# Performance work log

Measured on AMD Instinct MI355X. Metric: run time of the kernel, lower is better.

Reference implementation:

```python
import jax, jax.numpy as jnp
import numpy as np

N_NODES = 50000; N_INTRA = 800000; N_INTER = 400000; N_IEDGE = 600000
N_GRAPHS = 128; F_IN = 54; DIM = 128; N_GNN = 3; DIM_MLP = 128
DEV_VDW_COEFF = 0.2; EPS_LO = 0.0178; EPS_HI = 0.2
VDW_N_SHORT = 10.0; VDW_N_LONG = 6.0
RANGE_LO = 0.5; RANGE_HI = 5.0
HBOND_CUT = (-0.7, 0.0); METAL_CUT = (-0.7, 0.0); HYDRO_CUT = (0.5, 1.5)


def _lin(key, fi, fo):
    return jax.random.normal(key, (fi, fo), jnp.float32) / np.float32(np.sqrt(fi))


def setup_inputs():
    key = jax.random.key(0)
    ks = iter(jax.random.split(key, 48))
    nk = lambda: next(ks)
    inp = {}
    inp['x'] = jax.random.normal(nk(), (N_NODES, F_IN), jnp.float32)
    inp['pos'] = jax.random.uniform(nk(), (N_NODES, 3), jnp.float32, 0.0, 20.0)
    inp['vdw_radii'] = jax.random.uniform(nk(), (N_NODES,), jnp.float32, 1.0, 2.0)
    inp['rotor'] = jax.random.randint(nk(), (N_GRAPHS, 1), 0, 20).astype(jnp.float32)
    inp['edge_index'] = jax.random.randint(nk(), (2, N_INTRA), 0, N_NODES)
    inp['edge_index_c'] = jax.random.randint(nk(), (2, N_INTER), 0, N_NODES)
    inp['edge_index_i'] = jax.random.randint(nk(), (2, N_IEDGE), 0, N_NODES)
    inp['batch'] = jnp.sort(jax.random.randint(nk(), (N_NODES,), 0, N_GRAPHS))
    for name, p in (('is_metal', 0.02), ('is_h_donor', 0.15), ('is_h_acceptor', 0.2), ('is_hydrophobic', 0.4)):
        inp[name] = jax.random.bernoulli(nk(), p, (N_NODES,))
    inp['embed_W'] = _lin(nk(), F_IN, DIM)
    inp['gat_W'] = jax.random.normal(nk(), (N_GNN, DIM, DIM), jnp.float32) / np.float32(np.sqrt(DIM))
    inp['gat_Wb'] = jnp.zeros((N_GNN, DIM), jnp.float32)
    inp['gat_A'] = 0.1 * jax.random.normal(nk(), (N_GNN, DIM, DIM), jnp.float32) / np.float32(np.sqrt(DIM))
    inp['gat_gate_w'] = jax.random.normal(nk(), (N_GNN, 2 * DIM, 1), jnp.float32) / np.float32(np.sqrt(2 * DIM))
    inp['gat_gate_b'] = jnp.zeros((N_GNN, 1), jnp.float32)
    inp['inter_W'] = jax.random.normal(nk(), (N_GNN, DIM, DIM), jnp.float32) / np.float32(np.sqrt(DIM))
    inp['inter_Wb'] = jnp.zeros((N_GNN, DIM), jnp.float32)
    inp['inter_gate_w'] = jax.random.normal(nk(), (N_GNN, 2 * DIM, 1), jnp.float32) / np.float32(np.sqrt(2 * DIM))
    inp['inter_gate_b'] = jnp.zeros((N_GNN, 1), jnp.float32)
    inp['eps_w1'] = _lin(nk(), 2 * DIM, DIM_MLP); inp['eps_b1'] = jnp.zeros((DIM_MLP,), jnp.float32)
    inp['eps_w2'] = _lin(nk(), DIM_MLP, 1); inp['eps_b2'] = jnp.zeros((1,), jnp.float32)
    inp['dvdw_w1'] = _lin(nk(), 2 * DIM, DIM_MLP); inp['dvdw_b1'] = jnp.zeros((DIM_MLP,), jnp.float32)
    inp['dvdw_w2'] = _lin(nk(), DIM_MLP, 1); inp['dvdw_b2'] = jnp.zeros((1,), jnp.float32)
    inp['hbond_coeff'] = jnp.array([1.0], jnp.float32)
    inp['hydrophobic_coeff'] = jnp.array([0.5], jnp.float32)
    inp['rotor_coeff'] = jnp.array([0.5], jnp.float32)
    return inp


def _gated_gat(x, src, dst, W, Wb, A, gw, gb):
    n = x.shape[0]
    h = x @ W + Wb                                   # [N, D]
    logits = jnp.sum((h @ A)[dst] * h[src], axis=-1)  # per-edge attention logit
    mx = jax.ops.segment_max(logits, dst, num_segments=n)
    mx = jnp.where(jnp.isfinite(mx), mx, 0.0)
    ex = jnp.exp(logits - mx[dst])
    den = jax.ops.segment_sum(ex, dst, num_segments=n)
    alpha = ex / (den[dst] + 1e-16)                  # segment softmax over incoming edges
    h_prime = jax.nn.relu(jax.ops.segment_sum(alpha[:, None] * h[src], dst, num_segments=n))
    z = jax.nn.sigmoid(jnp.concatenate([x, h_prime], -1) @ gw + gb)
    return z * x + (1.0 - z) * h_prime


def _interaction(x, src, dst, W, Wb, gw, gb):
    n = x.shape[0]
    m = jax.ops.segment_sum(jax.nn.relu(x[src] @ W + Wb), dst, num_segments=n)
    z = jax.nn.sigmoid(jnp.concatenate([x, m], -1) @ gw + gb)
    return z * x + (1.0 - z) * m


def _lj(D, R, eps, n_short, n_long):
    dr = jnp.maximum(D / R, 0.5)  # numerical clamp mirroring PIGNet's distance clamp
    n = jnp.where(dr < 1.0, n_short, n_long)
    return eps * (dr ** (-2.0 * n) - 2.0 * dr ** (-n))


def _linear_potential(D, R, minima, c_short, c_long):
    frac = jnp.clip(((D - R) - c_long) / (c_short - c_long), 0.0, 1.0)
    return minima * frac


def _forward(x, pos, vdw_radii, rotor, embed_W, gat_W, gat_Wb, gat_A, gat_gate_w, gat_gate_b,
             inter_W, inter_Wb, inter_gate_w, inter_gate_b,
             eps_w1, eps_b1, eps_w2, eps_b2, dvdw_w1, dvdw_b1, dvdw_w2, dvdw_b2,
             hbond_coeff, hydrophobic_coeff, rotor_coeff,
             edge_index, edge_index_c, edge_index_i, batch,
             is_metal, is_h_donor, is_h_acceptor, is_hydrophobic):
    h = x @ embed_W
    for l in range(N_GNN):
        h = _gated_gat(h, edge_index[0], edge_index[1], gat_W[l], gat_Wb[l], gat_A[l], gat_gate_w[l], gat_gate_b[l])
    for l in range(N_GNN):
        h = _interaction(h, edge_index_c[0], edge_index_c[1], inter_W[l], inter_Wb[l], inter_gate_w[l], inter_gate_b[l])
    i, j = edge_index_i[0], edge_index_i[1]
    diff = pos[i] - pos[j]
    D = jnp.sqrt(jnp.sum(diff * diff, axis=-1) + 1e-10)           # [E]
    rmask = ((D >= RANGE_LO) & (D <= RANGE_HI)).astype(h.dtype)
    x_cat = jnp.concatenate([h[i], h[j]], axis=-1)                # [E, 2*DIM]
    dvdw = jnp.tanh(jax.nn.relu(x_cat @ dvdw_w1 + dvdw_b1) @ dvdw_w2 + dvdw_b2)[:, 0]
    dvdw = dvdw * DEV_VDW_COEFF * rmask
    R = vdw_radii[i] + vdw_radii[j] + dvdw
    eps = jax.nn.sigmoid(jax.nn.relu(x_cat @ eps_w1 + eps_b1) @ eps_w2 + eps_b2)[:, 0]
    eps = eps * (EPS_HI - EPS_LO) + EPS_LO
    min_hb = -hbond_coeff ** 2
    min_hp = -hydrophobic_coeff ** 2
    e = jnp.stack([
        _lj(D, R, eps, VDW_N_SHORT, VDW_N_LONG),
        _linear_potential(D, R, min_hb, *HBOND_CUT),
        _linear_potential(D, R, min_hb, *METAL_CUT),
        _linear_potential(D, R, min_hp, *HYDRO_CUT),
    ])                                                            # [4, E]
    no_metal = ~(is_metal[i] | is_metal[j])
    masks = jnp.stack([
        no_metal,
        ((is_h_donor[i] & is_h_acceptor[j]) | (is_h_acceptor[i] & is_h_donor[j])) & no_metal,
        (is_metal[i] & is_h_acceptor[j]) | (is_h_acceptor[i] & is_metal[j]),
        is_hydrophobic[i] & is_hydrophobic[j] & no_metal,
    ]).astype(e.dtype)
    e = e * masks * rmask
    energies = jax.ops.segment_sum(e.T, batch[i], num_segments=N_GRAPHS)  # [G, 4]
    penalty = 1.0 + rotor_coeff ** 2 * rotor                               # [G, 1]
    return energies / penalty, dvdw


def reference(x, pos, vdw_radii, rotor, edge_index, edge_index_c, edge_index_i, batch,
              is_metal, is_h_donor, is_h_acceptor, is_hydrophobic,
              embed_W, gat_W, gat_Wb, gat_A, gat_gate_w, gat_gate_b,
              inter_W, inter_Wb, inter_gate_w, inter_gate_b,
              eps_w1, eps_b1, eps_w2, eps_b2, dvdw_w1, dvdw_b1, dvdw_w2, dvdw_b2,
              hbond_coeff, hydrophobic_coeff, rotor_coeff):
    return _forward(x, pos, vdw_radii, rotor, embed_W, gat_W, gat_Wb, gat_A, gat_gate_w, gat_gate_b,
                    inter_W, inter_Wb, inter_gate_w, inter_gate_b,
                    eps_w1, eps_b1, eps_w2, eps_b2, dvdw_w1, dvdw_b1, dvdw_w2, dvdw_b2,
                    hbond_coeff, hydrophobic_coeff, rotor_coeff,
                    edge_index, edge_index_c, edge_index_i, batch,
                    is_metal, is_h_donor, is_h_acceptor, is_hydrophobic)
```

## Files before the change

kernel.cpp:

```cpp
#include <hip/hip_runtime.h>
#include <math.h>

#define NN 50000
#define EA 800000
#define EC 400000
#define EIN 600000
#define NG 128
#define FIN 54

#define DEV_VDW 0.2f
#define EPS_LO_ 0.0178f
#define EPS_HI_ 0.2f

typedef unsigned int uint;
typedef unsigned short ushort;
typedef unsigned long long ull;
typedef __attribute__((ext_vector_type(8))) short bf16x8;
typedef __attribute__((ext_vector_type(4))) float f32x4;

__device__ __forceinline__ ushort f2bf(float f){
  uint x = __float_as_uint(f);
  uint r = x + 0x7fffu + ((x >> 16) & 1u);
  return (ushort)(r >> 16);
}
__device__ __forceinline__ uint f2bf2(float a, float b){
  return (uint)f2bf(a) | ((uint)f2bf(b) << 16);
}
__device__ __forceinline__ void decode8(uint4 u, float* f){
  f[0] = __uint_as_float(u.x << 16); f[1] = __uint_as_float(u.x & 0xffff0000u);
  f[2] = __uint_as_float(u.y << 16); f[3] = __uint_as_float(u.y & 0xffff0000u);
  f[4] = __uint_as_float(u.z << 16); f[5] = __uint_as_float(u.z & 0xffff0000u);
  f[6] = __uint_as_float(u.w << 16); f[7] = __uint_as_float(u.w & 0xffff0000u);
}

__global__ void k_rank(const int* __restrict__ dstA, const int* __restrict__ dstC,
                       const int* __restrict__ dstI,
                       int* __restrict__ cntA, int* __restrict__ cntC, int* __restrict__ cntI,
                       int* __restrict__ rnkA, int* __restrict__ rnkC, int* __restrict__ rnkI){
  int b = blockIdx.x;
  const int* dst; int* cnt; int* rnk; int E; int bid; int nb;
  if (b < 1024){ dst = dstA; cnt = cntA; rnk = rnkA; E = EA;  bid = b;        nb = 1024; }
  else if (b < 1536){ dst = dstC; cnt = cntC; rnk = rnkC; E = EC;  bid = b - 1024; nb = 512; }
  else { dst = dstI; cnt = cntI; rnk = rnkI; E = EIN; bid = b - 1536; nb = 1024; }
  for (int i = bid * 256 + threadIdx.x; i < E; i += nb * 256)
    rnk[i] = atomicAdd(&cnt[dst[i]], 1);
}

__global__ void k_scan3(const int* __restrict__ cntA, int* __restrict__ offA,
                        const int* __restrict__ cntC, int* __restrict__ offC,
                        const int* __restrict__ cntI, int* __restrict__ offI){
  const int* cnt = (blockIdx.x == 0) ? cntA : (blockIdx.x == 1) ? cntC : cntI;
  int* off = (blockIdx.x == 0) ? offA : (blockIdx.x == 1) ? offC : offI;
  int n = NN;
  __shared__ int wsums[16];
  __shared__ int run_s;
  int tid = threadIdx.x;
  int lane = tid & 63, w = tid >> 6;
  if (tid == 0) run_s = 0;
  __syncthreads();
  for (int base = 0; base < n; base += 1024){
    int run = run_s;
    int i = base + tid;
    int v = (i < n) ? cnt[i] : 0;
    int s = v;
    #pragma unroll
    for (int o = 1; o < 64; o <<= 1){ int t = __shfl_up(s, o, 64); if (lane >= o) s += t; }
    if (lane == 63) wsums[w] = s;
    __syncthreads();
    if (w == 0 && lane < 16){
      int t = wsums[lane];
      #pragma unroll
      for (int o = 1; o < 16; o <<= 1){ int u = __shfl_up(t, o, 64); if (lane >= o) t += u; }
      wsums[lane] = t;
    }
    __syncthreads();
    int woff = (w == 0) ? 0 : wsums[w - 1];
    int excl = run + woff + (s - v);
    if (i < n) off[i] = excl;
    int tot = wsums[15];
    __syncthreads();
    if (tid == 0) run_s = run + tot;
    __syncthreads();
  }
  if (threadIdx.x == 0) off[n] = run_s;
}

__global__ void k_place(const int* __restrict__ eiA, const int* __restrict__ eiC,
                        const int* __restrict__ eiI,
                        const int* __restrict__ offA, const int* __restrict__ rnkA, int* __restrict__ srcA,
                        const int* __restrict__ offC, const int* __restrict__ rnkC, int* __restrict__ srcC,
                        const int* __restrict__ offI, const int* __restrict__ rnkI, ull* __restrict__ jeI){
  int b = blockIdx.x;
  if (b < 1024){
    for (int i = b * 256 + threadIdx.x; i < EA; i += 1024 * 256){
      int d = eiA[EA + i];
      __builtin_nontemporal_store(eiA[i], &srcA[offA[d] + rnkA[i]]);
    }
  } else if (b < 1536){
    int bid = b - 1024;
    for (int i = bid * 256 + threadIdx.x; i < EC; i += 512 * 256){
      int d = eiC[EC + i];
      __builtin_nontemporal_store(eiC[i], &srcC[offC[d] + rnkC[i]]);
    }
  } else {
    int bid = b - 1536;
    for (int i = bid * 256 + threadIdx.x; i < EIN; i += 1024 * 256){
      int key = eiI[i];
      ull v = ((ull)(uint)i << 32) | (uint)eiI[EIN + i];
      __builtin_nontemporal_store(v, &jeI[offI[key] + rnkI[i]]);
    }
  }
}

__global__ void k_nodeinfo(const float* __restrict__ POS, const float* __restrict__ RAD,
                           const int* __restrict__ Mmet, const int* __restrict__ Mdon,
                           const int* __restrict__ Macc, const int* __restrict__ Mhyd,
                           const int* __restrict__ BATCH,
                           float4* __restrict__ PRAD, uint* __restrict__ MB){
  int n = blockIdx.x * 256 + threadIdx.x;
  if (n < NN){
    PRAD[n] = make_float4(POS[3*n], POS[3*n+1], POS[3*n+2], RAD[n]);
    uint m = (Mmet[n] ? 1u : 0u) | (Mdon[n] ? 2u : 0u) | (Macc[n] ? 4u : 0u) |
             (Mhyd[n] ? 8u : 0u) | ((uint)BATCH[n] << 8);
    MB[n] = m;
  }
}

__global__ __launch_bounds__(256) void k_prepw(const float* __restrict__ gatW, const float* __restrict__ gatA,
                        const float* __restrict__ intW, const float* __restrict__ dw1,
                        const float* __restrict__ ew1,
                        const float* __restrict__ gatWb, const float* __restrict__ intWb,
                        const float* __restrict__ db1, const float* __restrict__ eb1,
                        uint* __restrict__ Wt, float* __restrict__ BIASALL){
  __shared__ ushort L[128 * 132];
  int m = blockIdx.x;
  int tid = threadIdx.x;
  if (m == 13){
    for (int idx = tid; idx < 13 * 128; idx += 256){
      int slot = idx >> 7, c = idx & 127;
      if (slot >= 3 && slot < 6) continue;
      float v = 0.f;
      if (slot < 3) v = gatWb[slot * 128 + c];
      else if (slot < 9) v = intWb[(slot - 6) * 128 + c];
      else if (slot == 9) v = db1[c];
      else if (slot == 11) v = eb1[c];
      BIASALL[idx] = v;
    }
    return;
  }
  if (m >= 3 && m < 6){
    int l = m - 3;
    const float* Wf  = gatW + l * 16384;
    const float* Af  = gatA + l * 16384;
    const float* Wbf = gatWb + l * 128;
    for (int idx = tid; idx < 16384; idx += 256){
      int k = idx >> 7, n = idx & 127;
      L[k * 132 + n] = f2bf(Af[idx]);
    }
    __syncthreads();
    int r = tid >> 1, ch = tid & 1;
    float accv[64];
    #pragma unroll
    for (int c = 0; c < 64; ++c) accv[c] = 0.f;
    float accb = 0.f;
    int bc = tid & 127;
    for (int mm = 0; mm < 128; ++mm){
      float wv = Wf[r * 128 + mm];
      const uint* Lr32 = (const uint*)&L[mm * 132 + ch * 64];
      #pragma unroll
      for (int c2 = 0; c2 < 32; ++c2){
        uint u = Lr32[c2];
        accv[2 * c2]     += wv * __uint_as_float(u << 16);
        accv[2 * c2 + 1] += wv * __uint_as_float(u & 0xffff0000u);
      }
      accb += Wbf[mm] * __uint_as_float((uint)L[mm * 132 + bc] << 16);
    }
    __syncthreads();
    #pragma unroll
    for (int c = 0; c < 64; ++c) L[r * 132 + ch * 64 + c] = f2bf(accv[c]);
    if (tid < 128) BIASALL[(3 + l) * 128 + tid] = accb;
    __syncthreads();
    int n = tid & 127, half = tid >> 7;
    uint* outp = Wt + (size_t)m * 8192 + n * 64 + half * 32;
    #pragma unroll
    for (int kk2 = 0; kk2 < 32; ++kk2){
      int k = half * 64 + 2 * kk2;
      uint u = (uint)L[k * 132 + n] | ((uint)L[(k + 1) * 132 + n] << 16);
      outp[kk2] = u;
    }
    return;
  }
  const float* src = (m < 3)  ? gatW + m * 16384 :
                     (m < 9)  ? intW + (m - 6) * 16384 :
                     (m < 11) ? dw1 + (m - 9) * 16384 :
                                ew1 + (m - 11) * 16384;
  for (int idx = tid; idx < 16384; idx += 256){
    int k = idx >> 7, n = idx & 127;
    L[k * 132 + n] = f2bf(src[idx]);
  }
  __syncthreads();
  int n = tid & 127, half = tid >> 7;
  uint* outp = Wt + (size_t)m * 8192 + n * 64 + half * 32;
  #pragma unroll
  for (int kk2 = 0; kk2 < 32; ++kk2){
    int k = half * 64 + 2 * kk2;
    uint u = (uint)L[k * 132 + n] | ((uint)L[(k + 1) * 132 + n] << 16);
    outp[kk2] = u;
  }
}

__global__ void k_embed(const float* __restrict__ X, const float* __restrict__ W,
                        uint* __restrict__ Hh){
  __shared__ float Wls[FIN * 128];
  int tid = threadIdx.x;
  for (int i = tid; i < FIN * 128; i += 128) Wls[i] = W[i];
  __syncthreads();
  for (int row = blockIdx.x; row < NN; row += gridDim.x){
    const float* xr = X + row * FIN;
    float acc = 0.f;
    #pragma unroll
    for (int k = 0; k < FIN; ++k) acc += xr[k] * Wls[k * 128 + tid];
    ((ushort*)Hh)[(size_t)row * 128 + tid] = f2bf(acc);
  }
}

template<bool RELU>
__global__ __launch_bounds__(256) void k_gemm_mfma(const uint* __restrict__ Ah,
        const uint* __restrict__ Bt0, size_t strideB,
        const float* __restrict__ bias0, size_t strideBias,
        uint* __restrict__ C0, size_t strideC, int N){
  const uint* Bt = Bt0 + (size_t)blockIdx.y * strideB;
  const float* bias = bias0 + (size_t)blockIdx.y * strideBias;
  uint* Cout = C0 + (size_t)blockIdx.y * strideC;
  int tid = threadIdx.x;
  int lane = tid & 63;
  int wv = tid >> 6;
  int row0 = blockIdx.x * 128 + wv * 32;
  int l15 = lane & 15, lg = lane >> 4;
  int ra0 = row0 + l15, ra1 = row0 + 16 + l15;
  const uint* pa0 = Ah + (size_t)(ra0 < N ? ra0 : 0) * 64 + lg * 4;
  const uint* pa1 = Ah + (size_t)(ra1 < N ? ra1 : 0) * 64 + lg * 4;
  const uint* pb  = Bt + (size_t)l15 * 64 + lg * 4;
  f32x4 acc[2][8] = {};
  #pragma unroll
  for (int c = 0; c < 4; ++c){
    bf16x8 a0 = *(const bf16x8*)(pa0 + c * 16);
    bf16x8 a1 = *(const bf16x8*)(pa1 + c * 16);
    #pragma unroll
    for (int ct = 0; ct < 8; ++ct){
      bf16x8 b = *(const bf16x8*)(pb + ct * 1024 + c * 16);
      acc[0][ct] = __builtin_amdgcn_mfma_f32_16x16x32_bf16(a0, b, acc[0][ct], 0, 0, 0);
      acc[1][ct] = __builtin_amdgcn_mfma_f32_16x16x32_bf16(a1, b, acc[1][ct], 0, 0, 0);
    }
  }
  #pragma unroll
  for (int ct = 0; ct < 8; ++ct){
    int col = ct * 16 + l15;
    float bv = bias[col];
    #pragma unroll
    for (int rt = 0; rt < 2; ++rt){
      int rbase = row0 + rt * 16 + lg * 4;
      f32x4 a4 = acc[rt][ct];
      #pragma unroll
      for (int r = 0; r < 4; ++r){
        int row = rbase + r;
        if (row < N){
          float t = a4[r] + bv;
          if (RELU) t = fmaxf(t, 0.f);
          ((ushort*)Cout)[(size_t)row * 128 + col] = f2bf(t);
        }
      }
    }
  }
}

__global__ __launch_bounds__(256) void k_gat(uint* __restrict__ Hh,
                      const uint* __restrict__ HWh, const uint* __restrict__ HAh,
                      const int* __restrict__ off, const int* __restrict__ srcs,
                      const float* __restrict__ GW, const float* __restrict__ GB){
  int tid = threadIdx.x;
  int sub = tid & 15;
  int n = blockIdx.x * 16 + (tid >> 4);
  if (n >= NN) return;
  uint4 au = *(const uint4*)(HAh + (size_t)n * 64 + sub * 4);
  float a[8]; decode8(au, a);
  int e0 = off[n], deg = off[n + 1] - e0;
  float m = -INFINITY, den = 0.f;
  float acc[8] = {};
  uint4 w0v = {}, w1v = {}, w2v = {};
  if (deg > 0) w0v = *(const uint4*)(HWh + (size_t)srcs[e0] * 64 + sub * 4);
  if (deg > 1) w1v = *(const uint4*)(HWh + (size_t)srcs[e0 + 1] * 64 + sub * 4);
  if (deg > 2) w2v = *(const uint4*)(HWh + (size_t)srcs[e0 + 2] * 64 + sub * 4);
  for (int t = 0; t < deg; ++t){
    uint4 wn = {};
    if (t + 3 < deg) wn = *(const uint4*)(HWh + (size_t)srcs[e0 + t + 3] * 64 + sub * 4);
    float w[8]; decode8(w0v, w);
    float p = a[0]*w[0] + a[1]*w[1] + a[2]*w[2] + a[3]*w[3]
            + a[4]*w[4] + a[5]*w[5] + a[6]*w[6] + a[7]*w[7];
    #pragma unroll
    for (int o = 8; o; o >>= 1) p += __shfl_xor(p, o, 64);
    float mn = fmaxf(m, p);
    float cf = __expf(m - mn);
    float ex = __expf(p - mn);
    den = den * cf + ex;
    #pragma unroll
    for (int q = 0; q < 8; ++q) acc[q] = acc[q] * cf + ex * w[q];
    m = mn;
    w0v = w1v; w1v = w2v; w2v = wn;
  }
  float inv = 1.f / (den + 1e-16f);
  float hp[8];
  #pragma unroll
  for (int q = 0; q < 8; ++q) hp[q] = fmaxf(acc[q] * inv, 0.f);
  uint4 xu = *(const uint4*)(Hh + (size_t)n * 64 + sub * 4);
  float x[8]; decode8(xu, x);
  float gx[8], gh[8];
  *(float4*)&gx[0] = *(const float4*)(GW + sub * 8);
  *(float4*)&gx[4] = *(const float4*)(GW + sub * 8 + 4);
  *(float4*)&gh[0] = *(const float4*)(GW + 128 + sub * 8);
  *(float4*)&gh[4] = *(const float4*)(GW + 128 + sub * 8 + 4);
  float g = 0.f;
  #pragma unroll
  for (int q = 0; q < 8; ++q) g += x[q] * gx[q] + hp[q] * gh[q];
  #pragma unroll
  for (int o = 8; o; o >>= 1) g += __shfl_xor(g, o, 64);
  g += GB[0];
  float z = 1.f / (1.f + __expf(-g));
  #pragma unroll
  for (int q = 0; q < 8; ++q) x[q] = z * x[q] + (1.f - z) * hp[q];
  uint4 hw;
  hw.x = f2bf2(x[0], x[1]); hw.y = f2bf2(x[2], x[3]);
  hw.z = f2bf2(x[4], x[5]); hw.w = f2bf2(x[6], x[7]);
  *(uint4*)(Hh + (size_t)n * 64 + sub * 4) = hw;
}

__global__ __launch_bounds__(256) void k_inter(uint* __restrict__ Hh,
                        const uint* __restrict__ Th,
                        const int* __restrict__ off, const int* __restrict__ srcs,
                        const float* __restrict__ GW, const float* __restrict__ GB){
  int tid = threadIdx.x;
  int sub = tid & 15;
  int n = blockIdx.x * 16 + (tid >> 4);
  if (n >= NN) return;
  int e0 = off[n], deg = off[n + 1] - e0;
  float acc[8] = {};
  uint4 w0v = {}, w1v = {}, w2v = {};
  if (deg > 0) w0v = *(const uint4*)(Th + (size_t)srcs[e0] * 64 + sub * 4);
  if (deg > 1) w1v = *(const uint4*)(Th + (size_t)srcs[e0 + 1] * 64 + sub * 4);
  if (deg > 2) w2v = *(const uint4*)(Th + (size_t)srcs[e0 + 2] * 64 + sub * 4);
  for (int t = 0; t < deg; ++t){
    uint4 wn = {};
    if (t + 3 < deg) wn = *(const uint4*)(Th + (size_t)srcs[e0 + t + 3] * 64 + sub * 4);
    float w[8]; decode8(w0v, w);
    #pragma unroll
    for (int q = 0; q < 8; ++q) acc[q] += w[q];
    w0v = w1v; w1v = w2v; w2v = wn;
  }
  uint4 xu = *(const uint4*)(Hh + (size_t)n * 64 + sub * 4);
  float x[8]; decode8(xu, x);
  float gx[8], gh[8];
  *(float4*)&gx[0] = *(const float4*)(GW + sub * 8);
  *(float4*)&gx[4] = *(const float4*)(GW + sub * 8 + 4);
  *(float4*)&gh[0] = *(const float4*)(GW + 128 + sub * 8);
  *(float4*)&gh[4] = *(const float4*)(GW + 128 + sub * 8 + 4);
  float g = 0.f;
  #pragma unroll
  for (int q = 0; q < 8; ++q) g += x[q] * gx[q] + acc[q] * gh[q];
  #pragma unroll
  for (int o = 8; o; o >>= 1) g += __shfl_xor(g, o, 64);
  g += GB[0];
  float z = 1.f / (1.f + __expf(-g));
  #pragma unroll
  for (int q = 0; q < 8; ++q) x[q] = z * x[q] + (1.f - z) * acc[q];
  uint4 hw;
  hw.x = f2bf2(x[0], x[1]); hw.y = f2bf2(x[2], x[3]);
  hw.z = f2bf2(x[4], x[5]); hw.w = f2bf2(x[6], x[7]);
  *(uint4*)(Hh + (size_t)n * 64 + sub * 4) = hw;
}

__global__ __launch_bounds__(256) void k_edges(
    const int* __restrict__ offI, const ull* __restrict__ jeI,
    const float4* __restrict__ PRAD, const uint* __restrict__ MB,
    const uint* __restrict__ Pd, const uint* __restrict__ Qd,
    const uint* __restrict__ Pe, const uint* __restrict__ Qe,
    const float* __restrict__ w2d, const float* __restrict__ b2d,
    const float* __restrict__ w2e, const float* __restrict__ b2e,
    const float* __restrict__ hbc, const float* __restrict__ hpc,
    float* __restrict__ geng, float* __restrict__ outdv){
  int tid = threadIdx.x;
  int sub = tid & 15;
  int n = blockIdx.x * 16 + (tid >> 4);
  if (n >= NN) return;
  int e0 = offI[n], deg = offI[n + 1] - e0;
  if (deg == 0) return;
  float wdv[8], wev[8];
  *(float4*)&wdv[0] = *(const float4*)(w2d + sub * 8);
  *(float4*)&wdv[4] = *(const float4*)(w2d + sub * 8 + 4);
  *(float4*)&wev[0] = *(const float4*)(w2e + sub * 8);
  *(float4*)&wev[4] = *(const float4*)(w2e + sub * 8 + 4);
  float bd = b2d[0], be = b2e[0];
  float minhb = -hbc[0] * hbc[0], minhp = -hpc[0] * hpc[0];
  uint4 pdu = *(const uint4*)(Pd + (size_t)n * 64 + sub * 4);
  uint4 peu = *(const uint4*)(Pe + (size_t)n * 64 + sub * 4);
  float pdf[8], pef[8];
  decode8(pdu, pdf); decode8(peu, pef);
  float4 pri = PRAD[n];
  uint mbi = MB[n];
  float E0 = 0.f, E1 = 0.f, E2 = 0.f, E3 = 0.f;

  ull je0 = jeI[e0];
  int j0 = (int)(uint)je0;
  uint4 qd0 = *(const uint4*)(Qd + (size_t)j0 * 64 + sub * 4);
  uint4 qe0 = *(const uint4*)(Qe + (size_t)j0 * 64 + sub * 4);
  float4 prj0 = PRAD[j0];
  uint mbj0 = MB[j0];

  for (int t = 0; t < deg; ++t){
    ull je1 = 0; uint4 qd1 = {}, qe1 = {}; float4 prj1 = {}; uint mbj1 = 0;
    if (t + 1 < deg){
      je1 = jeI[e0 + t + 1];
      int j1 = (int)(uint)je1;
      qd1 = *(const uint4*)(Qd + (size_t)j1 * 64 + sub * 4);
      qe1 = *(const uint4*)(Qe + (size_t)j1 * 64 + sub * 4);
      prj1 = PRAD[j1]; mbj1 = MB[j1];
    }
    float qdf[8], qef[8];
    decode8(qd0, qdf); decode8(qe0, qef);
    float sd = 0.f, se = 0.f;
    #pragma unroll
    for (int q = 0; q < 8; ++q){
      sd += fmaxf(pdf[q] + qdf[q], 0.f) * wdv[q];
      se += fmaxf(pef[q] + qef[q], 0.f) * wev[q];
    }
    #pragma unroll
    for (int o = 8; o; o >>= 1){
      sd += __shfl_xor(sd, o, 64);
      se += __shfl_xor(se, o, 64);
    }
    sd += bd; se += be;
    float dx = pri.x - prj0.x, dy = pri.y - prj0.y, dz = pri.z - prj0.z;
    float D = sqrtf(dx * dx + dy * dy + dz * dz + 1e-10f);
    float rmask = (D >= 0.5f && D <= 5.0f) ? 1.f : 0.f;
    float ex2 = __expf(2.f * fminf(sd, 15.f));
    float th = __fdividef(ex2 - 1.f, ex2 + 1.f);
    float dvdw = th * DEV_VDW * rmask;
    float eps = __fdividef(1.f, 1.f + __expf(-se)) * (EPS_HI_ - EPS_LO_) + EPS_LO_;
    float R = pri.w + prj0.w + dvdw;
    float dr = fmaxf(__fdividef(D, R), 0.5f);
    float nn2 = (dr < 1.f) ? 10.f : 6.f;
    float tp = __expf(-nn2 * __logf(dr));
    float ev = eps * (tp * tp - 2.f * tp);
    float dmr = D - R;
    float f1 = fminf(fmaxf(dmr * (-1.f / 0.7f), 0.f), 1.f);
    float f3 = fminf(fmaxf(1.5f - dmr, 0.f), 1.f);
    bool metI = mbi & 1, metJ = mbj0 & 1;
    bool donI = mbi & 2, donJ = mbj0 & 2;
    bool accI = mbi & 4, accJ = mbj0 & 4;
    bool hyI  = mbi & 8, hyJ  = mbj0 & 8;
    bool nm = !(metI || metJ);
    if (sub == 0) __builtin_nontemporal_store(dvdw, &outdv[(int)(je0 >> 32)]);
    E0 += nm ? ev * rmask : 0.f;
    E1 += (((donI && accJ) || (accI && donJ)) && nm) ? minhb * f1 * rmask : 0.f;
    E2 += ((metI && accJ) || (accI && metJ)) ? minhb * f1 * rmask : 0.f;
    E3 += (hyI && hyJ && nm) ? minhp * f3 * rmask : 0.f;
    je0 = je1; qd0 = qd1; qe0 = qe1; prj0 = prj1; mbj0 = mbj1;
  }
  if (sub == 0){
    float* part = geng + (size_t)(blockIdx.x & 7) * (NG * 4);
    int g = (int)(mbi >> 8) * 4;
    atomicAdd(&part[g + 0], E0);
    atomicAdd(&part[g + 1], E1);
    atomicAdd(&part[g + 2], E2);
    atomicAdd(&part[g + 3], E3);
  }
}

__global__ void k_final(const float* __restrict__ geng, const float* __restrict__ rotor,
                        const float* __restrict__ rc, float* __restrict__ out){
  int t = blockIdx.x * blockDim.x + threadIdx.x;
  if (t < NG * 4){
    int g = t >> 2;
    float s = 0.f;
    #pragma unroll
    for (int p = 0; p < 8; ++p) s += geng[p * NG * 4 + t];
    float pen = 1.f + rc[0] * rc[0] * rotor[g];
    out[t] = s / pen;
  }
}

extern "C" void kernel_launch(void* const* d_in, const int* in_sizes, int n_in,
                              void* d_out, int out_size, void* d_ws, size_t ws_size,
                              hipStream_t stream){
  (void)in_sizes; (void)n_in; (void)out_size; (void)ws_size;
  const float* X    = (const float*)d_in[0];
  const float* POS  = (const float*)d_in[1];
  const float* RAD  = (const float*)d_in[2];
  const float* ROT  = (const float*)d_in[3];
  const int* EIa    = (const int*)d_in[4];
  const int* EIc    = (const int*)d_in[5];
  const int* EIi    = (const int*)d_in[6];
  const int* BATCH  = (const int*)d_in[7];
  const int* Mmet = (const int*)d_in[8];
  const int* Mdon = (const int*)d_in[9];
  const int* Macc = (const int*)d_in[10];
  const int* Mhyd = (const int*)d_in[11];
  const float* embW  = (const float*)d_in[12];
  const float* gatW  = (const float*)d_in[13];
  const float* gatWb = (const float*)d_in[14];
  const float* gatA  = (const float*)d_in[15];
  const float* gatGw = (const float*)d_in[16];
  const float* gatGb = (const float*)d_in[17];
  const float* intW  = (const float*)d_in[18];
  const float* intWb = (const float*)d_in[19];
  const float* intGw = (const float*)d_in[20];
  const float* intGb = (const float*)d_in[21];
  const float* ew1 = (const float*)d_in[22];
  const float* eb1 = (const float*)d_in[23];
  const float* ew2 = (const float*)d_in[24];
  const float* eb2 = (const float*)d_in[25];
  const float* dw1 = (const float*)d_in[26];
  const float* db1 = (const float*)d_in[27];
  const float* dw2 = (const float*)d_in[28];
  const float* db2 = (const float*)d_in[29];
  const float* hbc = (const float*)d_in[30];
  const float* hpc = (const float*)d_in[31];
  const float* rcc = (const float*)d_in[32];
  float* out = (float*)d_out;

  char* w = (char*)d_ws;
  uint* Hh   = (uint*)w;  w += (size_t)NN * 64 * 4;
  uint* BAh  = (uint*)w;  w += (size_t)NN * 64 * 4;
  uint* BBh  = (uint*)w;  w += (size_t)NN * 64 * 4;
  uint* Peh  = (uint*)w;  w += (size_t)NN * 64 * 4;
  uint* Qeh  = (uint*)w;  w += (size_t)NN * 64 * 4;
  uint* WT   = (uint*)w;  w += (size_t)13 * 8192 * 4;
  float* BIASALL = (float*)w; w += (size_t)13 * 128 * 4;
  float4* PRAD = (float4*)w; w += (size_t)NN * 16;
  uint* MBb  = (uint*)w;  w += (size_t)NN * 4;
  float* GENG = (float*)w; w += (size_t)8 * 512 * 4;
  int* cntA = (int*)w; w += (size_t)NN * 4;
  int* offA = (int*)w; w += (size_t)(NN + 1) * 4;
  int* srcA = (int*)w; w += (size_t)EA * 4;
  int* rnkA = (int*)w; w += (size_t)EA * 4;
  int* cntC = (int*)w; w += (size_t)NN * 4;
  int* offC = (int*)w; w += (size_t)(NN + 1) * 4;
  int* srcC = (int*)w; w += (size_t)EC * 4;
  int* rnkC = (int*)w; w += (size_t)EC * 4;
  int* cntI = (int*)w; w += (size_t)NN * 4;
  int* offI = (int*)w; w += (size_t)(NN + 1) * 4;
  int* rnkI = (int*)w; w += (size_t)EIN * 4;
  ull* jeI  = (ull*)w; w += (size_t)EIN * 8;
  uint* Th  = BAh;
  uint* Pdh = BAh;
  uint* Qdh = BBh;

  hipMemsetAsync(cntA, 0, (size_t)NN * 4, stream);
  hipMemsetAsync(cntC, 0, (size_t)NN * 4, stream);
  hipMemsetAsync(cntI, 0, (size_t)NN * 4, stream);
  hipMemsetAsync(GENG, 0, (size_t)8 * 512 * 4, stream);

  k_rank<<<2560, 256, 0, stream>>>(EIa + EA, EIc + EC, EIi, cntA, cntC, cntI, rnkA, rnkC, rnkI);
  k_scan3<<<3, 1024, 0, stream>>>(cntA, offA, cntC, offC, cntI, offI);
  k_place<<<2560, 256, 0, stream>>>(EIa, EIc, EIi, offA, rnkA, srcA, offC, rnkC, srcC, offI, rnkI, jeI);

  k_prepw<<<14, 256, 0, stream>>>(gatW, gatA, intW, dw1, ew1, gatWb, intWb, db1, eb1, WT, BIASALL);
  k_nodeinfo<<<(NN + 255) / 256, 256, 0, stream>>>(POS, RAD, Mmet, Mdon, Macc, Mhyd, BATCH, PRAD, MBb);
  k_embed<<<2048, 128, 0, stream>>>(X, embW, Hh);

  int gg = (NN + 127) / 128;
  int nodeGrid = (NN + 15) / 16;
  for (int l = 0; l < 3; ++l){
    k_gemm_mfma<false><<<dim3(gg, 2), 256, 0, stream>>>(Hh, WT + (size_t)l * 8192, (size_t)3 * 8192,
                                                        BIASALL + l * 128, (size_t)3 * 128,
                                                        BAh, (size_t)NN * 64, NN);
    k_gat<<<nodeGrid, 256, 0, stream>>>(Hh, BAh, BBh, offA, srcA, gatGw + l * 256, gatGb + l);
  }
  for (int l = 0; l < 3; ++l){
    k_gemm_mfma<true><<<dim3(gg, 1), 256, 0, stream>>>(Hh, WT + (size_t)(6 + l) * 8192, 0,
                                                       BIASALL + (6 + l) * 128, 0, Th, 0, NN);
    k_inter<<<nodeGrid, 256, 0, stream>>>(Hh, Th, offC, srcC, intGw + l * 256, intGb + l);
  }
  k_gemm_mfma<false><<<dim3(gg, 4), 256, 0, stream>>>(Hh, WT + (size_t)9 * 8192, (size_t)8192,
                                                      BIASALL + 9 * 128, (size_t)128,
                                                      BAh, (size_t)NN * 64, NN);

  k_edges<<<nodeGrid, 256, 0, stream>>>(offI, jeI, PRAD, MBb, Pdh, Qdh, Peh, Qeh,
                                        dw2, db2, ew2, eb2, hbc, hpc,
                                        GENG, out + 512);
  k_final<<<2, 256, 0, stream>>>(GENG, ROT, rcc, out);
}
```

Before: 889.0 us.

## Process interaction edges directly instead of building a CSR by source node

Drops the counting-sort/CSR construction for the interaction edge list (rank, scan, place) and has k_edges walk the raw edge list with a grid-stride loop and software prefetch. Per-edge energies now go to shared-memory per-graph accumulators, which are flushed to global memory once per block. The three zeroing memsets are merged into one. This removes three passes over the 600k edges, but every edge must now gather the source node's P features as well, instead of loading them once per node, and there are more shared atomics.

```diff
diff --git a/kernel.cpp b/kernel.cpp
--- a/kernel.cpp
+++ b/kernel.cpp
@@ -34,23 +34,23 @@
 }
 
 __global__ void k_rank(const int* __restrict__ dstA, const int* __restrict__ dstC,
-                       const int* __restrict__ dstI,
-                       int* __restrict__ cntA, int* __restrict__ cntC, int* __restrict__ cntI,
-                       int* __restrict__ rnkA, int* __restrict__ rnkC, int* __restrict__ rnkI){
+                       int* __restrict__ cntA, int* __restrict__ cntC,
+                       int* __restrict__ rnkA, int* __restrict__ rnkC){
   int b = blockIdx.x;
-  const int* dst; int* cnt; int* rnk; int E; int bid; int nb;
-  if (b < 1024){ dst = dstA; cnt = cntA; rnk = rnkA; E = EA;  bid = b;        nb = 1024; }
-  else if (b < 1536){ dst = dstC; cnt = cntC; rnk = rnkC; E = EC;  bid = b - 1024; nb = 512; }
-  else { dst = dstI; cnt = cntI; rnk = rnkI; E = EIN; bid = b - 1536; nb = 1024; }
-  for (int i = bid * 256 + threadIdx.x; i < E; i += nb * 256)
-    rnk[i] = atomicAdd(&cnt[dst[i]], 1);
-}
-
-__global__ void k_scan3(const int* __restrict__ cntA, int* __restrict__ offA,
-                        const int* __restrict__ cntC, int* __restrict__ offC,
-                        const int* __restrict__ cntI, int* __restrict__ offI){
-  const int* cnt = (blockIdx.x == 0) ? cntA : (blockIdx.x == 1) ? cntC : cntI;
-  int* off = (blockIdx.x == 0) ? offA : (blockIdx.x == 1) ? offC : offI;
+  if (b < 1024){
+    for (int i = b * 256 + threadIdx.x; i < EA; i += 1024 * 256)
+      rnkA[i] = atomicAdd(&cntA[dstA[i]], 1);
+  } else {
+    int bid = b - 1024;
+    for (int i = bid * 256 + threadIdx.x; i < EC; i += 512 * 256)
+      rnkC[i] = atomicAdd(&cntC[dstC[i]], 1);
+  }
+}
+
+__global__ void k_scan2(const int* __restrict__ cntA, int* __restrict__ offA,
+                        const int* __restrict__ cntC, int* __restrict__ offC){
+  const int* cnt = blockIdx.x ? cntC : cntA;
+  int* off = blockIdx.x ? offC : offA;
   int n = NN;
   __shared__ int wsums[16];
   __shared__ int run_s;
@@ -86,28 +86,19 @@
 }
 
 __global__ void k_place(const int* __restrict__ eiA, const int* __restrict__ eiC,
-                        const int* __restrict__ eiI,
                         const int* __restrict__ offA, const int* __restrict__ rnkA, int* __restrict__ srcA,
-                        const int* __restrict__ offC, const int* __restrict__ rnkC, int* __restrict__ srcC,
-                        const int* __restrict__ offI, const int* __restrict__ rnkI, ull* __restrict__ jeI){
+                        const int* __restrict__ offC, const int* __restrict__ rnkC, int* __restrict__ srcC){
   int b = blockIdx.x;
   if (b < 1024){
     for (int i = b * 256 + threadIdx.x; i < EA; i += 1024 * 256){
       int d = eiA[EA + i];
       __builtin_nontemporal_store(eiA[i], &srcA[offA[d] + rnkA[i]]);
     }
-  } else if (b < 1536){
+  } else {
     int bid = b - 1024;
     for (int i = bid * 256 + threadIdx.x; i < EC; i += 512 * 256){
       int d = eiC[EC + i];
       __builtin_nontemporal_store(eiC[i], &srcC[offC[d] + rnkC[i]]);
-    }
-  } else {
-    int bid = b - 1536;
-    for (int i = bid * 256 + threadIdx.x; i < EIN; i += 1024 * 256){
-      int key = eiI[i];
-      ull v = ((ull)(uint)i << 32) | (uint)eiI[EIN + i];
-      __builtin_nontemporal_store(v, &jeI[offI[key] + rnkI[i]]);
     }
   }
 }
@@ -379,7 +370,7 @@
 }
 
 __global__ __launch_bounds__(256) void k_edges(
-    const int* __restrict__ offI, const ull* __restrict__ jeI,
+    const int* __restrict__ EI,
     const float4* __restrict__ PRAD, const uint* __restrict__ MB,
     const uint* __restrict__ Pd, const uint* __restrict__ Qd,
     const uint* __restrict__ Pe, const uint* __restrict__ Qe,
@@ -387,12 +378,13 @@
     const float* __restrict__ w2e, const float* __restrict__ b2e,
     const float* __restrict__ hbc, const float* __restrict__ hpc,
     float* __restrict__ geng, float* __restrict__ outdv){
-  int tid = threadIdx.x;
+  __shared__ float eg[NG * 4];
+  int tid = threadIdx.x;
+  for (int i = tid; i < NG * 4; i += 256) eg[i] = 0.f;
+  __syncthreads();
   int sub = tid & 15;
-  int n = blockIdx.x * 16 + (tid >> 4);
-  if (n >= NN) return;
-  int e0 = offI[n], deg = offI[n + 1] - e0;
-  if (deg == 0) return;
+  int gid = blockIdx.x * 16 + (tid >> 4);
+  int ngrp = gridDim.x * 16;
   float wdv[8], wev[8];
   *(float4*)&wdv[0] = *(const float4*)(w2d + sub * 8);
   *(float4*)&wdv[4] = *(const float4*)(w2d + sub * 8 + 4);
@@ -400,32 +392,38 @@
   *(float4*)&wev[4] = *(const float4*)(w2e + sub * 8 + 4);
   float bd = b2d[0], be = b2e[0];
   float minhb = -hbc[0] * hbc[0], minhp = -hpc[0] * hpc[0];
-  uint4 pdu = *(const uint4*)(Pd + (size_t)n * 64 + sub * 4);
-  uint4 peu = *(const uint4*)(Pe + (size_t)n * 64 + sub * 4);
-  float pdf[8], pef[8];
-  decode8(pdu, pdf); decode8(peu, pef);
-  float4 pri = PRAD[n];
-  uint mbi = MB[n];
-  float E0 = 0.f, E1 = 0.f, E2 = 0.f, E3 = 0.f;
-
-  ull je0 = jeI[e0];
-  int j0 = (int)(uint)je0;
-  uint4 qd0 = *(const uint4*)(Qd + (size_t)j0 * 64 + sub * 4);
-  uint4 qe0 = *(const uint4*)(Qe + (size_t)j0 * 64 + sub * 4);
-  float4 prj0 = PRAD[j0];
-  uint mbj0 = MB[j0];
-
-  for (int t = 0; t < deg; ++t){
-    ull je1 = 0; uint4 qd1 = {}, qe1 = {}; float4 prj1 = {}; uint mbj1 = 0;
-    if (t + 1 < deg){
-      je1 = jeI[e0 + t + 1];
-      int j1 = (int)(uint)je1;
+
+  int e = gid;
+  uint4 pd0 = {}, qd0 = {}, pe0 = {}, qe0 = {};
+  float4 pri0 = {}, prj0 = {};
+  uint mbi0 = 0, mbj0 = 0;
+  int i1 = 0, j1 = 0;
+  if (e < EIN){
+    int i0 = EI[e], j0 = EI[EIN + e];
+    pd0 = *(const uint4*)(Pd + (size_t)i0 * 64 + sub * 4);
+    qd0 = *(const uint4*)(Qd + (size_t)j0 * 64 + sub * 4);
+    pe0 = *(const uint4*)(Pe + (size_t)i0 * 64 + sub * 4);
+    qe0 = *(const uint4*)(Qe + (size_t)j0 * 64 + sub * 4);
+    pri0 = PRAD[i0]; prj0 = PRAD[j0]; mbi0 = MB[i0]; mbj0 = MB[j0];
+  }
+  if (e + ngrp < EIN){ i1 = EI[e + ngrp]; j1 = EI[EIN + e + ngrp]; }
+
+  for (; e < EIN; e += ngrp){
+    uint4 pd1 = {}, qd1 = {}, pe1 = {}, qe1 = {};
+    float4 pri1 = {}, prj1 = {};
+    uint mbi1 = 0, mbj1 = 0;
+    int i2 = 0, j2 = 0;
+    if (e + ngrp < EIN){
+      pd1 = *(const uint4*)(Pd + (size_t)i1 * 64 + sub * 4);
       qd1 = *(const uint4*)(Qd + (size_t)j1 * 64 + sub * 4);
+      pe1 = *(const uint4*)(Pe + (size_t)i1 * 64 + sub * 4);
       qe1 = *(const uint4*)(Qe + (size_t)j1 * 64 + sub * 4);
-      prj1 = PRAD[j1]; mbj1 = MB[j1];
-    }
-    float qdf[8], qef[8];
-    decode8(qd0, qdf); decode8(qe0, qef);
+      pri1 = PRAD[i1]; prj1 = PRAD[j1]; mbi1 = MB[i1]; mbj1 = MB[j1];
+    }
+    if (e + 2 * ngrp < EIN){ i2 = EI[e + 2 * ngrp]; j2 = EI[EIN + e + 2 * ngrp]; }
+
+    float pdf[8], qdf[8], pef[8], qef[8];
+    decode8(pd0, pdf); decode8(qd0, qdf); decode8(pe0, pef); decode8(qe0, qef);
     float sd = 0.f, se = 0.f;
     #pragma unroll
     for (int q = 0; q < 8; ++q){
@@ -438,14 +436,14 @@
       se += __shfl_xor(se, o, 64);
     }
     sd += bd; se += be;
-    float dx = pri.x - prj0.x, dy = pri.y - prj0.y, dz = pri.z - prj0.z;
+    float dx = pri0.x - prj0.x, dy = pri0.y - prj0.y, dz = pri0.z - prj0.z;
     float D = sqrtf(dx * dx + dy * dy + dz * dz + 1e-10f);
     float rmask = (D >= 0.5f && D <= 5.0f) ? 1.f : 0.f;
     float ex2 = __expf(2.f * fminf(sd, 15.f));
     float th = __fdividef(ex2 - 1.f, ex2 + 1.f);
     float dvdw = th * DEV_VDW * rmask;
     float eps = __fdividef(1.f, 1.f + __expf(-se)) * (EPS_HI_ - EPS_LO_) + EPS_LO_;
-    float R = pri.w + prj0.w + dvdw;
+    float R = pri0.w + prj0.w + dvdw;
     float dr = fmaxf(__fdividef(D, R), 0.5f);
     float nn2 = (dr < 1.f) ? 10.f : 6.f;
     float tp = __expf(-nn2 * __logf(dr));
@@ -453,26 +451,30 @@
     float dmr = D - R;
     float f1 = fminf(fmaxf(dmr * (-1.f / 0.7f), 0.f), 1.f);
     float f3 = fminf(fmaxf(1.5f - dmr, 0.f), 1.f);
-    bool metI = mbi & 1, metJ = mbj0 & 1;
-    bool donI = mbi & 2, donJ = mbj0 & 2;
-    bool accI = mbi & 4, accJ = mbj0 & 4;
-    bool hyI  = mbi & 8, hyJ  = mbj0 & 8;
+    bool metI = mbi0 & 1, metJ = mbj0 & 1;
+    bool donI = mbi0 & 2, donJ = mbj0 & 2;
+    bool accI = mbi0 & 4, accJ = mbj0 & 4;
+    bool hyI  = mbi0 & 8, hyJ  = mbj0 & 8;
     bool nm = !(metI || metJ);
-    if (sub == 0) __builtin_nontemporal_store(dvdw, &outdv[(int)(je0 >> 32)]);
-    E0 += nm ? ev * rmask : 0.f;
-    E1 += (((donI && accJ) || (accI && donJ)) && nm) ? minhb * f1 * rmask : 0.f;
-    E2 += ((metI && accJ) || (accI && metJ)) ? minhb * f1 * rmask : 0.f;
-    E3 += (hyI && hyJ && nm) ? minhp * f3 * rmask : 0.f;
-    je0 = je1; qd0 = qd1; qe0 = qe1; prj0 = prj1; mbj0 = mbj1;
-  }
-  if (sub == 0){
-    float* part = geng + (size_t)(blockIdx.x & 7) * (NG * 4);
-    int g = (int)(mbi >> 8) * 4;
-    atomicAdd(&part[g + 0], E0);
-    atomicAdd(&part[g + 1], E1);
-    atomicAdd(&part[g + 2], E2);
-    atomicAdd(&part[g + 3], E3);
-  }
+    float E0 = nm ? ev * rmask : 0.f;
+    float E1 = (((donI && accJ) || (accI && donJ)) && nm) ? minhb * f1 * rmask : 0.f;
+    float E2 = ((metI && accJ) || (accI && metJ)) ? minhb * f1 * rmask : 0.f;
+    float E3 = (hyI && hyJ && nm) ? minhp * f3 * rmask : 0.f;
+    if (sub == 0){
+      outdv[e] = dvdw;
+      int g = (int)(mbi0 >> 8) * 4;
+      atomicAdd(&eg[g + 0], E0);
+      atomicAdd(&eg[g + 1], E1);
+      atomicAdd(&eg[g + 2], E2);
+      atomicAdd(&eg[g + 3], E3);
+    }
+    pd0 = pd1; qd0 = qd1; pe0 = pe1; qe0 = qe1;
+    pri0 = pri1; prj0 = prj1; mbi0 = mbi1; mbj0 = mbj1;
+    i1 = i2; j1 = j2;
+  }
+  __syncthreads();
+  float* part = geng + (size_t)(blockIdx.x & 7) * (NG * 4);
+  for (int i2 = tid; i2 < NG * 4; i2 += 256) atomicAdd(&part[i2], eg[i2]);
 }
 
 __global__ void k_final(const float* __restrict__ geng, const float* __restrict__ rotor,
@@ -537,31 +539,25 @@
   float* BIASALL = (float*)w; w += (size_t)13 * 128 * 4;
   float4* PRAD = (float4*)w; w += (size_t)NN * 16;
   uint* MBb  = (uint*)w;  w += (size_t)NN * 4;
+  int* cntA = (int*)w; w += (size_t)NN * 4;
+  int* cntC = (int*)w; w += (size_t)NN * 4;
   float* GENG = (float*)w; w += (size_t)8 * 512 * 4;
-  int* cntA = (int*)w; w += (size_t)NN * 4;
+  size_t zero_bytes = (size_t)2 * NN * 4 + (size_t)8 * 512 * 4;
   int* offA = (int*)w; w += (size_t)(NN + 1) * 4;
   int* srcA = (int*)w; w += (size_t)EA * 4;
   int* rnkA = (int*)w; w += (size_t)EA * 4;
-  int* cntC = (int*)w; w += (size_t)NN * 4;
   int* offC = (int*)w; w += (size_t)(NN + 1) * 4;
   int* srcC = (int*)w; w += (size_t)EC * 4;
   int* rnkC = (int*)w; w += (size_t)EC * 4;
-  int* cntI = (int*)w; w += (size_t)NN * 4;
-  int* offI = (int*)w; w += (size_t)(NN + 1) * 4;
-  int* rnkI = (int*)w; w += (size_t)EIN * 4;
-  ull* jeI  = (ull*)w; w += (size_t)EIN * 8;
   uint* Th  = BAh;
   uint* Pdh = BAh;
   uint* Qdh = BBh;
 
-  hipMemsetAsync(cntA, 0, (size_t)NN * 4, stream);
-  hipMemsetAsync(cntC, 0, (size_t)NN * 4, stream);
-  hipMemsetAsync(cntI, 0, (size_t)NN * 4, stream);
-  hipMemsetAsync(GENG, 0, (size_t)8 * 512 * 4, stream);
-
-  k_rank<<<2560, 256, 0, stream>>>(EIa + EA, EIc + EC, EIi, cntA, cntC, cntI, rnkA, rnkC, rnkI);
-  k_scan3<<<3, 1024, 0, stream>>>(cntA, offA, cntC, offC, cntI, offI);
-  k_place<<<2560, 256, 0, stream>>>(EIa, EIc, EIi, offA, rnkA, srcA, offC, rnkC, srcC, offI, rnkI, jeI);
+  hipMemsetAsync(cntA, 0, zero_bytes, stream);
+
+  k_rank<<<1536, 256, 0, stream>>>(EIa + EA, EIc + EC, cntA, cntC, rnkA, rnkC);
+  k_scan2<<<2, 1024, 0, stream>>>(cntA, offA, cntC, offC);
+  k_place<<<1536, 256, 0, stream>>>(EIa, EIc, offA, rnkA, srcA, offC, rnkC, srcC);
 
   k_prepw<<<14, 256, 0, stream>>>(gatW, gatA, intW, dw1, ew1, gatWb, intWb, db1, eb1, WT, BIASALL);
   k_nodeinfo<<<(NN + 255) / 256, 256, 0, stream>>>(POS, RAD, Mmet, Mdon, Macc, Mhyd, BATCH, PRAD, MBb);
@@ -584,8 +580,8 @@
                                                       BIASALL + 9 * 128, (size_t)128,
                                                       BAh, (size_t)NN * 64, NN);
 
-  k_edges<<<nodeGrid, 256, 0, stream>>>(offI, jeI, PRAD, MBb, Pdh, Qdh, Peh, Qeh,
-                                        dw2, db2, ew2, eb2, hbc, hpc,
-                                        GENG, out + 512);
+  k_edges<<<2048, 256, 0, stream>>>(EIi, PRAD, MBb, Pdh, Qdh, Peh, Qeh,
+                                    dw2, db2, ew2, eb2, hbc, hpc,
+                                    GENG, out + 512);
   k_final<<<2, 256, 0, stream>>>(GENG, ROT, rcc, out);
 }
```

Result: faster. 808.6 us (median of 2 runs) (-9.0%).
